# Kernel tuning notes

Measured on AMD Instinct MI355X. Metric: run time of the kernel, lower is better.

## Reference

```python
import jax, jax.numpy as jnp
import numpy as np

IMG = 64        # img_size
D_STEPS = 64    # cnfg['d_steps']
D_MAX = 1.0     # cnfg['d_max']


def _consts():
    f = 70.0 * (IMG / 64.0)
    c = IMG / 2.0 - 0.5
    K = jnp.array([[f, 0.0, c], [0.0, f, c], [0.0, 0.0, 1.0]], jnp.float32)
    K_inv = jnp.linalg.inv(K)
    R_t = jnp.eye(3, dtype=jnp.float32)          # transpose(cnfg['R']) with R=I
    t = jnp.array([[0.0], [0.0], [2.5]], jnp.float32)  # cnfg['t'][:,None]
    return K, K_inv, R_t, t


def _rot_mat(alphas):
    # get_rotation_mat: Z-axis rotation by pi*alpha, (BS,3,3)
    a = jnp.pi * alphas
    c, s = jnp.cos(a), jnp.sin(a)
    z, o = jnp.zeros_like(a), jnp.ones_like(a)
    return jnp.stack([
        jnp.stack([c, -s, z], -1),
        jnp.stack([s, c, z], -1),
        jnp.stack([z, z, o], -1)], -2)


def _pred_depth_from_samplegrid(sdfvalues, Z_coords):
    # sdfvalues: (BS,H,W,D,1), Z_coords: (BS,H,W,D)
    pnts_out = jnp.where(sdfvalues > 0.0, 1.0, -1.0)
    # sign change + -> - along depth axis (zero crossing entering the surface)
    zc = (pnts_out[..., :-1, :] - pnts_out[..., 1:, :] == 2.0).astype(sdfvalues.dtype)
    occ = jnp.max(zc, axis=-2)                       # (BS,H,W,1)
    Zc = Z_coords[..., None]                         # (BS,H,W,D,1)
    zeros = jnp.zeros_like(zc[..., 0:1, :])

    def helper(zcross):
        tmp = 100.0 * (1.0 - zcross)
        depth = jnp.min(Zc * zcross + tmp, axis=-2)
        sdf = jnp.sum(sdfvalues * zcross, axis=-2)
        return sdf, depth

    s1, d1 = helper(jnp.concatenate([zc, zeros], axis=-2))
    s2, d2 = helper(jnp.concatenate([zeros, zc], axis=-2))
    eps = 1e-06
    depth_pred = occ * (d1 - s1 / (s2 - s1 - eps) * (d2 - d1))
    return depth_pred, occ


def _render(z_shape, z_extr, W1, b1, W2, b2):
    K, K_inv, R_t, t = _consts()
    BS = z_shape.shape[0]
    # get_obj_trans
    s_obj = (1.0 / z_extr[:, 0]).reshape(BS, 1, 1, 1)
    t_obj = z_extr[:, 1:4].reshape(BS, 1, 3, 1)
    R_obj = _rot_mat(z_extr[:, 4])                   # (BS,3,3)
    s_inv = 1.0 / s_obj
    R_obj_inv = jnp.linalg.inv(R_obj)
    # bounding-box depth offset (mean camera-space depth of 9 bbox points)
    corners = jnp.array([[1., 1., 1.], [1., 1., -1.], [1., -1., 1.], [1., -1., -1.],
                         [-1., 1., 1.], [-1., 1., -1.], [-1., -1., 1.], [-1., -1., -1.],
                         [0., 0., 0.]], jnp.float32)
    Xbb = jnp.broadcast_to(corners[None, :, :, None], (BS, 9, 3, 1))
    Xbb = jnp.einsum('bij,bajk->baik', R_obj_inv, s_inv * Xbb) + t_obj
    Xbb = jnp.einsum('ij,bajk->baik', jnp.linalg.inv(R_t), Xbb) + t
    Xbb = jnp.einsum('ij,bajk->baik', K, Xbb)
    bb_depth = jnp.mean(Xbb[:, :, 2:3], axis=1, keepdims=True)  # (BS,1,1,1)
    # image coordinate grid (full image; bbox crop has data-dependent shape)
    xs = jnp.linspace(0.0, IMG - 1.0, IMG)
    zs = jnp.linspace(-D_MAX, D_MAX, D_STEPS)
    Xg, Yg, Zg = jnp.meshgrid(xs, xs, zs)            # 'xy' indexing, (IMG,IMG,D)
    n = IMG * IMG
    coords_2d = jnp.stack([Xg.reshape(-1), Yg.reshape(-1)], -1)  # (n*D,2)
    coords_2d = jnp.broadcast_to(coords_2d[None], (BS, n * D_STEPS, 2))
    Z = Zg.reshape(1, n, D_STEPS, 1) * s_inv + bb_depth          # (BS,n,D,1)
    depth = Z.reshape(BS, n * D_STEPS, 1)
    coords_3d = jnp.concatenate([coords_2d, jnp.ones_like(depth)], axis=-1)
    # trans_pnts: pixel+depth -> world -> object coords
    X = coords_3d[..., None]                                     # (BS,N,3,1)
    X = jnp.einsum('ij,bajk->baik', K_inv, X)
    X = jnp.einsum('ij,bajk->baik', R_t, depth[..., None] * X - t)
    X = s_obj * jnp.einsum('bij,bajk->baik', R_obj, X - t_obj)
    X = X[..., 0]                                                # (BS,N,3)
    # deepsdf stub MLP on concat([X, z_shape])
    zt = jnp.broadcast_to(z_shape[:, None, :], (BS, X.shape[1], z_shape.shape[-1]))
    feat = jnp.concatenate([X, zt], axis=-1)                     # (BS,N,64)
    h = jax.nn.relu(jnp.einsum('bnf,fh->bnh', feat, W1) + b1)
    sdf = jnp.tanh(jnp.einsum('bnh,ho->bno', h, W2) + b2)        # (BS,N,1)
    sdf = sdf.reshape(BS, IMG, IMG, D_STEPS, 1)
    Zc = Z.reshape(BS, IMG, IMG, D_STEPS)
    depth_pred, occ = _pred_depth_from_samplegrid(sdf, Zc)
    return depth_pred, occ


def setup_inputs() -> dict:
    key = jax.random.key(0)
    k1, k2, k3, k4 = jax.random.split(key, 4)
    BS, D_SH, H1 = 4, 61, 128
    z_shape = jax.random.normal(k1, (BS, D_SH), jnp.float32)
    u = jax.random.uniform(k2, (BS, 5), jnp.float32)
    # scale in [0.75,1.25), translations in [-0.25,0.25), alpha in [0,1)
    z_extr = jnp.concatenate([0.75 + 0.5 * u[:, 0:1],
                              0.5 * (u[:, 1:4] - 0.5),
                              u[:, 4:5]], axis=1)
    W1 = 0.3 * jax.random.normal(k3, (3 + D_SH, H1), jnp.float32)
    b1 = jnp.zeros((H1,), jnp.float32)
    W2 = 0.3 * jax.random.normal(k4, (H1, 1), jnp.float32)
    b2 = jnp.zeros((1,), jnp.float32)
    return {"z_shape": z_shape, "z_extr": z_extr, "W1": W1, "b1": b1, "W2": W2, "b2": b2}


def reference(z_shape, z_extr, W1, b1, W2, b2):
    return _render(z_shape, z_extr, W1, b1, W2, b2)
```

## Files before the change

kernel.cpp:

```cpp
#include <hip/hip_runtime.h>
#include <math.h>


#define N_RAYS (4 * 64 * 64)

__global__ __launch_bounds__(512) void precompute_cvec(
    const float* __restrict__ z_shape,
    const float* __restrict__ W1,
    const float* __restrict__ b1,
    float* __restrict__ cvec)
{
    int tid = blockIdx.x * blockDim.x + threadIdx.x;
    if (tid >= 4 * 128) return;
    int b = tid >> 7;
    int h = tid & 127;
    float acc = b1[h];
    #pragma unroll
    for (int f = 0; f < 61; ++f)
        acc = fmaf(z_shape[b * 61 + f], W1[(3 + f) * 128 + h], acc);
    cvec[tid] = acc;
}

__global__ __launch_bounds__(256) void render_kernel(
    const float* __restrict__ z_extr,
    const float* __restrict__ W1,
    const float* __restrict__ W2,
    const float* __restrict__ b2,
    const float* __restrict__ cvec,
    float* __restrict__ out)
{
    const int lane = threadIdx.x & 63;
    const int wave = __builtin_amdgcn_readfirstlane((int)(threadIdx.x >> 6));
    const int ray  = blockIdx.x * 4 + wave;
    const int b    = ray >> 12;
    const int rem  = ray & 4095;
    const int yi   = rem >> 6;
    const int xj   = rem & 63;

    const float scale = z_extr[b * 5 + 0];
    const float tx    = z_extr[b * 5 + 1];
    const float ty    = z_extr[b * 5 + 2];
    const float tz    = z_extr[b * 5 + 3];
    const float alpha = z_extr[b * 5 + 4];

    const float a  = 3.14159274101257324f * alpha;
    const float ca = cosf(a);
    const float sa = sinf(a);
    const float s_obj = 1.0f / scale;
    const float s_inv = 1.0f / s_obj;
    const float T = tz + 2.5f;

    const float step = 2.0f / 63.0f;
    const float zk  = -1.0f + (float)lane * step;
    const float Z   = zk * s_inv + T;
    const float zk1 = -1.0f + (float)(lane + 1) * step;
    const float Z1  = zk1 * s_inv + T;

    const float kf  = 1.0f / 70.0f;
    const float kc  = -(31.5f / 70.0f);
    const float u = fmaf((float)xj, kf, kc);
    const float v = fmaf((float)yi, kf, kc);

    const float qx = Z * u - tx;
    const float qy = Z * v - ty;
    const float qz = (Z - 2.5f) - tz;
    const float X0 = s_obj * (ca * qx - sa * qy);
    const float X1 = s_obj * (sa * qx + ca * qy);
    const float X2 = s_obj * qz;

    const float4* __restrict__ w0 = (const float4*)(W1);
    const float4* __restrict__ w1 = (const float4*)(W1 + 128);
    const float4* __restrict__ w2 = (const float4*)(W1 + 256);
    const float4* __restrict__ wc = (const float4*)(cvec + b * 128);
    const float4* __restrict__ wo = (const float4*)(W2);

    float acc = b2[0];
    #pragma unroll 8
    for (int q = 0; q < 32; ++q) {
        const float4 a0 = w0[q];
        const float4 a1 = w1[q];
        const float4 a2 = w2[q];
        const float4 cc = wc[q];
        const float4 ww = wo[q];
        float h0 = fmaxf(fmaf(X0, a0.x, fmaf(X1, a1.x, fmaf(X2, a2.x, cc.x))), 0.0f);
        float h1 = fmaxf(fmaf(X0, a0.y, fmaf(X1, a1.y, fmaf(X2, a2.y, cc.y))), 0.0f);
        float h2 = fmaxf(fmaf(X0, a0.z, fmaf(X1, a1.z, fmaf(X2, a2.z, cc.z))), 0.0f);
        float h3 = fmaxf(fmaf(X0, a0.w, fmaf(X1, a1.w, fmaf(X2, a2.w, cc.w))), 0.0f);
        acc = fmaf(h0, ww.x, acc);
        acc = fmaf(h1, ww.y, acc);
        acc = fmaf(h2, ww.z, acc);
        acc = fmaf(h3, ww.w, acc);
    }
    const float sdf = tanhf(acc);

    const unsigned long long mask  = __ballot(sdf > 0.0f);
    const unsigned long long cross = mask & ~(mask >> 1) & 0x7fffffffffffffffULL;

    const bool isC = (cross >> lane) & 1ULL;
    const float sdf_next = __shfl_down(sdf, 1, 64);

    float d1 = isC ? Z        : 100.0f;
    float d2 = isC ? Z1       : 100.0f;
    float s1 = isC ? sdf      : 0.0f;
    float s2 = isC ? sdf_next : 0.0f;

    #pragma unroll
    for (int m = 1; m < 64; m <<= 1) {
        d1 = fminf(d1, __shfl_xor(d1, m, 64));
        d2 = fminf(d2, __shfl_xor(d2, m, 64));
        s1 += __shfl_xor(s1, m, 64);
        s2 += __shfl_xor(s2, m, 64);
    }

    if (lane == 0) {
        float occ = (cross != 0ULL) ? 1.0f : 0.0f;
        float depth = 0.0f;
        if (cross != 0ULL)
            depth = d1 - s1 / (s2 - s1 - 1e-6f) * (d2 - d1);
        out[ray]          = depth;
        out[N_RAYS + ray] = occ;
    }
}

extern "C" void kernel_launch(void* const* d_in, const int* in_sizes, int n_in,
                              void* d_out, int out_size, void* d_ws, size_t ws_size,
                              hipStream_t stream) {
    const float* z_shape = (const float*)d_in[0];
    const float* z_extr  = (const float*)d_in[1];
    const float* W1      = (const float*)d_in[2];
    const float* b1      = (const float*)d_in[3];
    const float* W2      = (const float*)d_in[4];
    const float* b2      = (const float*)d_in[5];
    float* out  = (float*)d_out;
    float* cvec = (float*)d_ws;

    precompute_cvec<<<1, 512, 0, stream>>>(z_shape, W1, b1, cvec);
    render_kernel<<<N_RAYS / 4, 256, 0, stream>>>(z_extr, W1, W2, b2, cvec, out);
}
```

Measured before the change: 88.89 us.

## Fuse cvec precompute into render kernel, stage weights in LDS, use packed FMA

Removes the separate precompute kernel launch. Every block now recomputes the per-batch latent contribution (a 61-term dot product per hidden unit) and stages W1's coordinate rows, cvec and W2 in shared memory. The MLP inner loop switches to two-wide vector FMAs so the compiler can emit packed fp32 instructions. The cost is redundant per-block recompute of cvec plus a barrier in each of 4096 blocks.

```diff
diff --git a/kernel.cpp b/kernel.cpp
--- a/kernel.cpp
+++ b/kernel.cpp
@@ -4,33 +4,41 @@
 
 #define N_RAYS (4 * 64 * 64)
 
-__global__ __launch_bounds__(512) void precompute_cvec(
+typedef float v2f __attribute__((ext_vector_type(2)));
+
+static __device__ __forceinline__ v2f mk2(float a, float b) {
+    v2f r; r.x = a; r.y = b; return r;
+}
+
+__global__ __launch_bounds__(256, 4) void render_kernel(
     const float* __restrict__ z_shape,
+    const float* __restrict__ z_extr,
     const float* __restrict__ W1,
     const float* __restrict__ b1,
-    float* __restrict__ cvec)
-{
-    int tid = blockIdx.x * blockDim.x + threadIdx.x;
-    if (tid >= 4 * 128) return;
-    int b = tid >> 7;
-    int h = tid & 127;
-    float acc = b1[h];
-    #pragma unroll
-    for (int f = 0; f < 61; ++f)
-        acc = fmaf(z_shape[b * 61 + f], W1[(3 + f) * 128 + h], acc);
-    cvec[tid] = acc;
-}
-
-__global__ __launch_bounds__(256) void render_kernel(
-    const float* __restrict__ z_extr,
-    const float* __restrict__ W1,
     const float* __restrict__ W2,
     const float* __restrict__ b2,
-    const float* __restrict__ cvec,
     float* __restrict__ out)
 {
-    const int lane = threadIdx.x & 63;
-    const int wave = __builtin_amdgcn_readfirstlane((int)(threadIdx.x >> 6));
+    __shared__ float sW[640];
+    const int tid = threadIdx.x;
+    const int bb  = blockIdx.x >> 10;
+
+    sW[tid] = W1[tid];
+    if (tid < 128) {
+        sW[256 + tid] = W1[256 + tid];
+    } else {
+        const int h = tid - 128;
+        sW[512 + h] = W2[h];
+        float a = b1[h];
+        #pragma unroll 8
+        for (int f = 0; f < 61; ++f)
+            a = fmaf(z_shape[bb * 61 + f], W1[(3 + f) * 128 + h], a);
+        sW[384 + h] = a;
+    }
+    __syncthreads();
+
+    const int lane = tid & 63;
+    const int wave = __builtin_amdgcn_readfirstlane(tid >> 6);
     const int ray  = blockIdx.x * 4 + wave;
     const int b    = ray >> 12;
     const int rem  = ray & 4095;
@@ -68,28 +76,37 @@
     const float X1 = s_obj * (sa * qx + ca * qy);
     const float X2 = s_obj * qz;
 
-    const float4* __restrict__ w0 = (const float4*)(W1);
-    const float4* __restrict__ w1 = (const float4*)(W1 + 128);
-    const float4* __restrict__ w2 = (const float4*)(W1 + 256);
-    const float4* __restrict__ wc = (const float4*)(cvec + b * 128);
-    const float4* __restrict__ wo = (const float4*)(W2);
+    const float4* __restrict__ w0 = (const float4*)(sW);
+    const float4* __restrict__ w1 = (const float4*)(sW + 128);
+    const float4* __restrict__ w2 = (const float4*)(sW + 256);
+    const float4* __restrict__ wc = (const float4*)(sW + 384);
+    const float4* __restrict__ wo = (const float4*)(sW + 512);
+
+    const v2f X0v = mk2(X0, X0);
+    const v2f X1v = mk2(X1, X1);
+    const v2f X2v = mk2(X2, X2);
+    const v2f zero2 = mk2(0.0f, 0.0f);
 
     float acc = b2[0];
-    #pragma unroll 8
+    #pragma unroll 4
     for (int q = 0; q < 32; ++q) {
         const float4 a0 = w0[q];
         const float4 a1 = w1[q];
         const float4 a2 = w2[q];
         const float4 cc = wc[q];
         const float4 ww = wo[q];
-        float h0 = fmaxf(fmaf(X0, a0.x, fmaf(X1, a1.x, fmaf(X2, a2.x, cc.x))), 0.0f);
-        float h1 = fmaxf(fmaf(X0, a0.y, fmaf(X1, a1.y, fmaf(X2, a2.y, cc.y))), 0.0f);
-        float h2 = fmaxf(fmaf(X0, a0.z, fmaf(X1, a1.z, fmaf(X2, a2.z, cc.z))), 0.0f);
-        float h3 = fmaxf(fmaf(X0, a0.w, fmaf(X1, a1.w, fmaf(X2, a2.w, cc.w))), 0.0f);
-        acc = fmaf(h0, ww.x, acc);
-        acc = fmaf(h1, ww.y, acc);
-        acc = fmaf(h2, ww.z, acc);
-        acc = fmaf(h3, ww.w, acc);
+        v2f lo = __builtin_elementwise_fma(X2v, mk2(a2.x, a2.y), mk2(cc.x, cc.y));
+        lo = __builtin_elementwise_fma(X1v, mk2(a1.x, a1.y), lo);
+        lo = __builtin_elementwise_fma(X0v, mk2(a0.x, a0.y), lo);
+        lo = __builtin_elementwise_max(lo, zero2);
+        v2f hi = __builtin_elementwise_fma(X2v, mk2(a2.z, a2.w), mk2(cc.z, cc.w));
+        hi = __builtin_elementwise_fma(X1v, mk2(a1.z, a1.w), hi);
+        hi = __builtin_elementwise_fma(X0v, mk2(a0.z, a0.w), hi);
+        hi = __builtin_elementwise_max(hi, zero2);
+        acc = fmaf(lo.x, ww.x, acc);
+        acc = fmaf(lo.y, ww.y, acc);
+        acc = fmaf(hi.x, ww.z, acc);
+        acc = fmaf(hi.y, ww.w, acc);
     }
     const float sdf = tanhf(acc);
 
@@ -131,9 +148,8 @@
     const float* b1      = (const float*)d_in[3];
     const float* W2      = (const float*)d_in[4];
     const float* b2      = (const float*)d_in[5];
-    float* out  = (float*)d_out;
-    float* cvec = (float*)d_ws;
+    float* out = (float*)d_out;
 
-    precompute_cvec<<<1, 512, 0, stream>>>(z_shape, W1, b1, cvec);
-    render_kernel<<<N_RAYS / 4, 256, 0, stream>>>(z_extr, W1, W2, b2, cvec, out);
+    render_kernel<<<N_RAYS / 4, 256, 0, stream>>>(
+        z_shape, z_extr, W1, b1, W2, b2, out);
 }
```

Result: slower. 90.84 us (+2.2%).
